# Performance work log

Hardware: AMD Instinct MI355X
Metric: run time of the kernel (lower is better)

## Reference

```python
import jax, jax.numpy as jnp
import numpy as np

E, T, H, I = 8, 2048, 1024, 2048  # experts, tokens, hidden, intermediate


def setup_inputs() -> dict:
    key = jax.random.key(0)
    k1, k2, k3, k4, k5 = jax.random.split(key, 5)
    hiddens = jax.random.normal(k1, (T, H), dtype=jnp.float32)
    w1 = jax.random.normal(k2, (E, H, I), dtype=jnp.float32)  # gate proj
    w2 = jax.random.normal(k3, (E, I, H), dtype=jnp.float32)  # down proj
    w3 = jax.random.normal(k4, (E, H, I), dtype=jnp.float32)  # up proj
    # random partition of T tokens into E contiguous expert groups (sum == T)
    cuts = jnp.sort(jax.random.randint(k5, (E - 1,), 0, T + 1, dtype=jnp.int32))
    bounds = jnp.concatenate(
        [jnp.zeros((1,), jnp.int32), cuts, jnp.full((1,), T, jnp.int32)])
    batch_sizes = jnp.diff(bounds)  # [E], int32, sums to T
    return {"hiddens": hiddens, "w1_weight": w1, "w2_weight": w2,
            "w3_weight": w3, "batch_sizes": batch_sizes}


def reference(hiddens, w1_weight, w2_weight, w3_weight, batch_sizes):
    # grouped GEMM: tokens are contiguous per expert; group_sizes = batch_sizes
    up = jax.lax.ragged_dot(hiddens, w1_weight, batch_sizes)      # [T, I]
    up_r = jax.lax.ragged_dot(hiddens, w3_weight, batch_sizes)    # [T, I]
    gated = jax.nn.silu(up) * up_r                                # SiLU-gate fuse
    down = jax.lax.ragged_dot(gated, w2_weight, batch_sizes)      # [T, H]
    return down
```

## Files before the change

### kernel.cpp

```cpp
#include <hip/hip_runtime.h>
#include <hip/hip_bf16.h>
#include <stdint.h>


#define NE 8
#define NT 2048
#define NH 1024
#define NI 2048

typedef __attribute__((ext_vector_type(8))) short bh8;
typedef __attribute__((ext_vector_type(4))) short bh4;
typedef __attribute__((ext_vector_type(4))) float f32x4;
typedef __attribute__((ext_vector_type(2))) float f32x2;
typedef __attribute__((ext_vector_type(4))) float float4v;

#define BARRIER() asm volatile("s_waitcnt lgkmcnt(0)\n\ts_barrier" ::: "memory")

static __device__ __forceinline__ unsigned short f2bf(float f) {
  __hip_bfloat16 h = __float2bfloat16(f);
  return *reinterpret_cast<unsigned short*>(&h);
}

__global__ __launch_bounds__(256)
void cvt_h_kernel(const float* __restrict__ x, unsigned short* __restrict__ y) {
  int i = blockIdx.x * 256 + threadIdx.x;
  const float4v* xv = reinterpret_cast<const float4v*>(x);
  float4v a = xv[2 * i], b = xv[2 * i + 1];
  union { bh8 v; unsigned short u[8]; } o;
  o.u[0] = f2bf(a[0]); o.u[1] = f2bf(a[1]); o.u[2] = f2bf(a[2]); o.u[3] = f2bf(a[3]);
  o.u[4] = f2bf(b[0]); o.u[5] = f2bf(b[1]); o.u[6] = f2bf(b[2]); o.u[7] = f2bf(b[3]);
  reinterpret_cast<bh8*>(y)[i] = o.v;
}


__global__ __launch_bounds__(512, 2)
void moe_gemm1(const unsigned short* __restrict__ hb,
               const float* __restrict__ w1,
               const float* __restrict__ w3,
               const int* __restrict__ bsz,
               unsigned short* __restrict__ gated) {
  const int NWG = 2048;
  const int wg = (blockIdx.x & 7) * (NWG >> 3) + (blockIdx.x >> 3);
  const int mt = wg & 15;
  const int e = (wg >> 4) & 7;
  const int nt = wg >> 7;

  int off = 0;
#pragma unroll
  for (int j = 0; j < NE; ++j) { int v = bsz[j]; off += (j < e) ? v : 0; }
  const int te = bsz[e];
  if (mt * 128 >= te) return;

  const int tid = threadIdx.x;
  const int l = tid & 63, w = tid >> 6;
  const int wr = w >> 2, wc = w & 3;

  __shared__ __align__(16) unsigned short As[2][128 * 32];
  __shared__ __align__(16) unsigned short B1s[2][128 * 32];
  __shared__ __align__(16) unsigned short B3s[2][128 * 32];

  const int row0 = off + mt * 128;
  const int col0 = nt * 128;

  int gr = row0 + (tid >> 2); if (gr > NT - 1) gr = NT - 1;
  const unsigned short* agA = hb + (size_t)gr * NH + (tid & 3) * 8;
  const int awo = (tid >> 2) * 32 + (((tid & 3) ^ ((tid >> 3) & 3)) * 8);

  const int n0 = 2 * l;
  const float* w1p = w1 + (size_t)e * NH * NI + (size_t)(4 * w) * NI + (col0 + n0);
  const float* w3p = w3 + (size_t)e * NH * NI + (size_t)(4 * w) * NI + (col0 + n0);
  const int bwo = n0 * 32 + (((w >> 1) ^ (l & 3)) * 8) + (w & 1) * 4;

  const int arow = wr * 64 + (l & 15);
  const int fslA = ((l >> 4) ^ ((l >> 1) & 3)) * 8;
  const int nbase = wc * 32 + (l & 15);
  const int bsl = ((l >> 4) ^ ((nbase >> 1) & 3)) * 8;

  f32x4 acc1[4][2] = {};
  f32x4 acc3[4][2] = {};
  f32x2 rb1A[4], rb3A[4], rb1B[4], rb3B[4];
  bh8 rAA, rAB;

  auto issue = [&](int t, bh8& rA_, f32x2 (&rb1_)[4], f32x2 (&rb3_)[4]) {
    const int k0 = t * 32;
    rA_ = *(const bh8*)(agA + k0);
#pragma unroll
    for (int j = 0; j < 4; ++j) rb1_[j] = *(const f32x2*)(w1p + (size_t)(k0 + j) * NI);
#pragma unroll
    for (int j = 0; j < 4; ++j) rb3_[j] = *(const f32x2*)(w3p + (size_t)(k0 + j) * NI);
  };
  auto stage = [&](int b, bh8& rA_, f32x2 (&rb1_)[4], f32x2 (&rb3_)[4]) {
    *(bh8*)(&As[b][awo]) = rA_;
    bh4 q0, q1, r0, r1;
#pragma unroll
    for (int j = 0; j < 4; ++j) {
      q0[j] = (short)f2bf(rb1_[j][0]); q1[j] = (short)f2bf(rb1_[j][1]);
      r0[j] = (short)f2bf(rb3_[j][0]); r1[j] = (short)f2bf(rb3_[j][1]);
    }
    *(bh4*)(&B1s[b][bwo]) = q0;
    *(bh4*)(&B1s[b][bwo + 32]) = q1;
    *(bh4*)(&B3s[b][bwo]) = r0;
    *(bh4*)(&B3s[b][bwo + 32]) = r1;
  };
  auto mfma_step = [&](int b) {
    bh8 af[4];
#pragma unroll
    for (int m = 0; m < 4; ++m)
      af[m] = *(const bh8*)(&As[b][(arow + m * 16) * 32 + fslA]);
#pragma unroll
    for (int nf = 0; nf < 2; ++nf) {
      bh8 b1f = *(const bh8*)(&B1s[b][(nbase + nf * 16) * 32 + bsl]);
      bh8 b3f = *(const bh8*)(&B3s[b][(nbase + nf * 16) * 32 + bsl]);
#pragma unroll
      for (int m = 0; m < 4; ++m) {
        acc1[m][nf] = __builtin_amdgcn_mfma_f32_16x16x32_bf16(af[m], b1f, acc1[m][nf], 0, 0, 0);
        acc3[m][nf] = __builtin_amdgcn_mfma_f32_16x16x32_bf16(af[m], b3f, acc3[m][nf], 0, 0, 0);
      }
    }
  };

  issue(0, rAA, rb1A, rb3A);
  issue(1, rAB, rb1B, rb3B);
  stage(0, rAA, rb1A, rb3A);
  BARRIER();

#pragma unroll 1
  for (int u = 0; u < 16; ++u) {
    const int t0 = 2 * u;
    if (t0 + 2 < 32) issue(t0 + 2, rAA, rb1A, rb3A);
    mfma_step(0);
    stage(1, rAB, rb1B, rb3B);
    BARRIER();
    if (t0 + 3 < 32) issue(t0 + 3, rAB, rb1B, rb3B);
    mfma_step(1);
    if (t0 + 2 < 32) stage(0, rAA, rb1A, rb3A);
    BARRIER();
  }

#pragma unroll
  for (int m = 0; m < 4; ++m) {
#pragma unroll
    for (int r = 0; r < 4; ++r) {
      int trow = mt * 128 + wr * 64 + m * 16 + (l >> 4) * 4 + r;
      if (trow < te) {
        size_t base = (size_t)(off + trow) * NI + col0 + wc * 32 + (l & 15);
#pragma unroll
        for (int nf = 0; nf < 2; ++nf) {
          float u2 = acc1[m][nf][r];
          float g = acc3[m][nf][r];
          gated[base + nf * 16] = f2bf((u2 / (1.f + __expf(-u2))) * g);
        }
      }
    }
  }
}

__global__ __launch_bounds__(512, 2)
void moe_gemm2(const unsigned short* __restrict__ gated,
               const float* __restrict__ w2,
               const int* __restrict__ bsz,
               float* __restrict__ out) {
  const int NWG = 1024;
  const int wg = (blockIdx.x & 7) * (NWG >> 3) + (blockIdx.x >> 3);
  const int mt = wg & 15;
  const int e = (wg >> 4) & 7;
  const int nt = wg >> 7;

  int off = 0;
#pragma unroll
  for (int j = 0; j < NE; ++j) { int v = bsz[j]; off += (j < e) ? v : 0; }
  const int te = bsz[e];
  if (mt * 128 >= te) return;

  const int tid = threadIdx.x;
  const int l = tid & 63, w = tid >> 6;
  const int wr = w >> 2, wc = w & 3;

  __shared__ __align__(16) unsigned short As[2][128 * 32];
  __shared__ __align__(16) unsigned short Bs[2][128 * 32];

  const int row0 = off + mt * 128;
  const int col0 = nt * 128;

  int gr = row0 + (tid >> 2); if (gr > NT - 1) gr = NT - 1;
  const unsigned short* agA = gated + (size_t)gr * NI + (tid & 3) * 8;
  const int awo = (tid >> 2) * 32 + (((tid & 3) ^ ((tid >> 3) & 3)) * 8);

  const int n0 = 2 * l;
  const float* w2p = w2 + (size_t)e * NI * NH + (size_t)(4 * w) * NH + (col0 + n0);
  const int bwo = n0 * 32 + (((w >> 1) ^ (l & 3)) * 8) + (w & 1) * 4;

  const int arow = wr * 64 + (l & 15);
  const int fslA = ((l >> 4) ^ ((l >> 1) & 3)) * 8;
  const int nbase = wc * 32 + (l & 15);
  const int bsl = ((l >> 4) ^ ((nbase >> 1) & 3)) * 8;

  f32x4 acc[4][2] = {};
  f32x2 rbA[4], rbB[4];
  bh8 rAA, rAB;

  auto issue = [&](int t, bh8& rA_, f32x2 (&rb_)[4]) {
    const int k0 = t * 32;
    rA_ = *(const bh8*)(agA + k0);
#pragma unroll
    for (int j = 0; j < 4; ++j) rb_[j] = *(const f32x2*)(w2p + (size_t)(k0 + j) * NH);
  };
  auto stage = [&](int b, bh8& rA_, f32x2 (&rb_)[4]) {
    *(bh8*)(&As[b][awo]) = rA_;
    bh4 q0, q1;
#pragma unroll
    for (int j = 0; j < 4; ++j) {
      q0[j] = (short)f2bf(rb_[j][0]); q1[j] = (short)f2bf(rb_[j][1]);
    }
    *(bh4*)(&Bs[b][bwo]) = q0;
    *(bh4*)(&Bs[b][bwo + 32]) = q1;
  };
  auto mfma_step = [&](int b) {
    bh8 af[4];
#pragma unroll
    for (int m = 0; m < 4; ++m)
      af[m] = *(const bh8*)(&As[b][(arow + m * 16) * 32 + fslA]);
#pragma unroll
    for (int nf = 0; nf < 2; ++nf) {
      bh8 bf = *(const bh8*)(&Bs[b][(nbase + nf * 16) * 32 + bsl]);
#pragma unroll
      for (int m = 0; m < 4; ++m)
        acc[m][nf] = __builtin_amdgcn_mfma_f32_16x16x32_bf16(af[m], bf, acc[m][nf], 0, 0, 0);
    }
  };

  issue(0, rAA, rbA);
  issue(1, rAB, rbB);
  stage(0, rAA, rbA);
  BARRIER();

#pragma unroll 1
  for (int u = 0; u < 32; ++u) {
    const int t0 = 2 * u;
    if (t0 + 2 < 64) issue(t0 + 2, rAA, rbA);
    mfma_step(0);
    stage(1, rAB, rbB);
    BARRIER();
    if (t0 + 3 < 64) issue(t0 + 3, rAB, rbB);
    mfma_step(1);
    if (t0 + 2 < 64) stage(0, rAA, rbA);
    BARRIER();
  }

#pragma unroll
  for (int m = 0; m < 4; ++m) {
#pragma unroll
    for (int r = 0; r < 4; ++r) {
      int trow = mt * 128 + wr * 64 + m * 16 + (l >> 4) * 4 + r;
      if (trow < te) {
        size_t base = (size_t)(off + trow) * NH + col0 + wc * 32 + (l & 15);
#pragma unroll
        for (int nf = 0; nf < 2; ++nf)
          out[base + nf * 16] = acc[m][nf][r];
      }
    }
  }
}

extern "C" void kernel_launch(void* const* d_in, const int* in_sizes, int n_in,
                              void* d_out, int out_size, void* d_ws, size_t ws_size,
                              hipStream_t stream) {
  const float* hiddens = (const float*)d_in[0];
  const float* w1 = (const float*)d_in[1];
  const float* w2 = (const float*)d_in[2];
  const float* w3 = (const float*)d_in[3];
  const int* bsz = (const int*)d_in[4];
  float* out = (float*)d_out;

  unsigned short* hb = (unsigned short*)d_ws;
  unsigned short* gated = hb + (size_t)NT * NH;

  cvt_h_kernel<<<dim3(NT * NH / 8 / 256), dim3(256), 0, stream>>>(hiddens, hb);
  moe_gemm1<<<dim3(2048), dim3(512), 0, stream>>>(hb, w1, w3, bsz, gated);
  moe_gemm2<<<dim3(1024), dim3(512), 0, stream>>>(gated, w2, bsz, out);
}
```

Before: 135.0 us.

## Deepen register prefetch pipeline to four stages and raise MFMA wave priority

Both grouped-GEMM kernels now keep four K-tiles of global loads in flight in registers instead of two, rotating through four register sets with an unrolled four-phase loop. The aim is to hide more global memory latency for the fp32 weight streams. The MFMA sections are also wrapped in s_setprio so matrix work is favoured over other waves' memory issue. The extra register sets raise VGPR pressure, which may cut occupancy or cause spills, especially in the gate/up kernel.

Result: no change. 133.1 us (-1.4%).

```diff
diff --git a/kernel.cpp b/kernel.cpp
--- a/kernel.cpp
+++ b/kernel.cpp
@@ -78,8 +78,9 @@
 
   f32x4 acc1[4][2] = {};
   f32x4 acc3[4][2] = {};
-  f32x2 rb1A[4], rb3A[4], rb1B[4], rb3B[4];
-  bh8 rAA, rAB;
+  bh8 rA0, rA1, rA2, rA3;
+  f32x2 r10[4], r11[4], r12[4], r13[4];
+  f32x2 r30[4], r31[4], r32[4], r33[4];
 
   auto issue = [&](int t, bh8& rA_, f32x2 (&rb1_)[4], f32x2 (&rb3_)[4]) {
     const int k0 = t * 32;
@@ -107,6 +108,7 @@
 #pragma unroll
     for (int m = 0; m < 4; ++m)
       af[m] = *(const bh8*)(&As[b][(arow + m * 16) * 32 + fslA]);
+    __builtin_amdgcn_s_setprio(1);
 #pragma unroll
     for (int nf = 0; nf < 2; ++nf) {
       bh8 b1f = *(const bh8*)(&B1s[b][(nbase + nf * 16) * 32 + bsl]);
@@ -117,25 +119,31 @@
         acc3[m][nf] = __builtin_amdgcn_mfma_f32_16x16x32_bf16(af[m], b3f, acc3[m][nf], 0, 0, 0);
       }
     }
-  };
-
-  issue(0, rAA, rb1A, rb3A);
-  issue(1, rAB, rb1B, rb3B);
-  stage(0, rAA, rb1A, rb3A);
+    __builtin_amdgcn_s_setprio(0);
+  };
+#define PHASE(P, RAI, R1I, R3I, RAS, R1S, R3S, LDSP)                    \
+  {                                                                     \
+    if ((P) + 4 < 32) issue((P) + 4, RAI, R1I, R3I);                    \
+    mfma_step(LDSP);                                                    \
+    if ((P) + 1 < 32) stage((LDSP) ^ 1, RAS, R1S, R3S);                 \
+    BARRIER();                                                          \
+  }
+
+  issue(0, rA0, r10, r30);
+  issue(1, rA1, r11, r31);
+  issue(2, rA2, r12, r32);
+  issue(3, rA3, r13, r33);
+  stage(0, rA0, r10, r30);
   BARRIER();
 
 #pragma unroll 1
-  for (int u = 0; u < 16; ++u) {
-    const int t0 = 2 * u;
-    if (t0 + 2 < 32) issue(t0 + 2, rAA, rb1A, rb3A);
-    mfma_step(0);
-    stage(1, rAB, rb1B, rb3B);
-    BARRIER();
-    if (t0 + 3 < 32) issue(t0 + 3, rAB, rb1B, rb3B);
-    mfma_step(1);
-    if (t0 + 2 < 32) stage(0, rAA, rb1A, rb3A);
-    BARRIER();
-  }
+  for (int p = 0; p < 32; p += 4) {
+    PHASE(p + 0, rA0, r10, r30, rA1, r11, r31, 0);
+    PHASE(p + 1, rA1, r11, r31, rA2, r12, r32, 1);
+    PHASE(p + 2, rA2, r12, r32, rA3, r13, r33, 0);
+    PHASE(p + 3, rA3, r13, r33, rA0, r10, r30, 1);
+  }
+#undef PHASE
 
 #pragma unroll
   for (int m = 0; m < 4; ++m) {
@@ -196,8 +204,8 @@
   const int bsl = ((l >> 4) ^ ((nbase >> 1) & 3)) * 8;
 
   f32x4 acc[4][2] = {};
-  f32x2 rbA[4], rbB[4];
-  bh8 rAA, rAB;
+  bh8 rA0, rA1, rA2, rA3;
+  f32x2 r0_[4], r1_[4], r2_[4], r3_[4];
 
   auto issue = [&](int t, bh8& rA_, f32x2 (&rb_)[4]) {
     const int k0 = t * 32;
@@ -220,6 +228,7 @@
 #pragma unroll
     for (int m = 0; m < 4; ++m)
       af[m] = *(const bh8*)(&As[b][(arow + m * 16) * 32 + fslA]);
+    __builtin_amdgcn_s_setprio(1);
 #pragma unroll
     for (int nf = 0; nf < 2; ++nf) {
       bh8 bf = *(const bh8*)(&Bs[b][(nbase + nf * 16) * 32 + bsl]);
@@ -227,25 +236,31 @@
       for (int m = 0; m < 4; ++m)
         acc[m][nf] = __builtin_amdgcn_mfma_f32_16x16x32_bf16(af[m], bf, acc[m][nf], 0, 0, 0);
     }
-  };
-
-  issue(0, rAA, rbA);
-  issue(1, rAB, rbB);
-  stage(0, rAA, rbA);
+    __builtin_amdgcn_s_setprio(0);
+  };
+#define PHASE2(P, RAI, RBI, RAS, RBS, LDSP)                             \
+  {                                                                     \
+    if ((P) + 4 < 64) issue((P) + 4, RAI, RBI);                         \
+    mfma_step(LDSP);                                                    \
+    if ((P) + 1 < 64) stage((LDSP) ^ 1, RAS, RBS);                      \
+    BARRIER();                                                          \
+  }
+
+  issue(0, rA0, r0_);
+  issue(1, rA1, r1_);
+  issue(2, rA2, r2_);
+  issue(3, rA3, r3_);
+  stage(0, rA0, r0_);
   BARRIER();
 
 #pragma unroll 1
-  for (int u = 0; u < 32; ++u) {
-    const int t0 = 2 * u;
-    if (t0 + 2 < 64) issue(t0 + 2, rAA, rbA);
-    mfma_step(0);
-    stage(1, rAB, rbB);
-    BARRIER();
-    if (t0 + 3 < 64) issue(t0 + 3, rAB, rbB);
-    mfma_step(1);
-    if (t0 + 2 < 64) stage(0, rAA, rbA);
-    BARRIER();
-  }
+  for (int p = 0; p < 64; p += 4) {
+    PHASE2(p + 0, rA0, r0_, rA1, r1_, 0);
+    PHASE2(p + 1, rA1, r1_, rA2, r2_, 1);
+    PHASE2(p + 2, rA2, r2_, rA3, r3_, 0);
+    PHASE2(p + 3, rA3, r3_, rA0, r0_, 1);
+  }
+#undef PHASE2
 
 #pragma unroll
   for (int m = 0; m < 4; ++m) {
```

## Split gate/up GEMM into separate workgroups and move SiLU-gate into down GEMM

Applied to the files above, without the earlier changes.

The first GEMM no longer computes both w1 and w3 products in one workgroup. It launches twice as many workgroups, each computing one projection and writing it unfused as bf16. The down-projection kernel now loads both intermediates and applies SiLU-gating while staging A into shared memory. This halves registers and LDS per workgroup in the up kernel, with s_setprio around MFMA blocks added. The cost is an extra T×I intermediate write and read, a second rounding to bf16 before the gate, and repeated exp work per down-projection column tile.

Measured after the change: 189.1 us. +40.1%, slower.

```diff
diff --git a/kernel.cpp b/kernel.cpp
--- a/kernel.cpp
+++ b/kernel.cpp
@@ -19,6 +19,9 @@
 static __device__ __forceinline__ unsigned short f2bf(float f) {
   __hip_bfloat16 h = __float2bfloat16(f);
   return *reinterpret_cast<unsigned short*>(&h);
+}
+static __device__ __forceinline__ float bf2f(short s) {
+  return __uint_as_float(((unsigned int)(unsigned short)s) << 16);
 }
 
 __global__ __launch_bounds__(256)
@@ -34,16 +37,18 @@
 
 
 __global__ __launch_bounds__(512, 2)
-void moe_gemm1(const unsigned short* __restrict__ hb,
-               const float* __restrict__ w1,
-               const float* __restrict__ w3,
-               const int* __restrict__ bsz,
-               unsigned short* __restrict__ gated) {
-  const int NWG = 2048;
+void moe_up(const unsigned short* __restrict__ hb,
+            const float* __restrict__ w1,
+            const float* __restrict__ w3,
+            const int* __restrict__ bsz,
+            unsigned short* __restrict__ up,
+            unsigned short* __restrict__ upr) {
+  const int NWG = 4096;
   const int wg = (blockIdx.x & 7) * (NWG >> 3) + (blockIdx.x >> 3);
   const int mt = wg & 15;
   const int e = (wg >> 4) & 7;
-  const int nt = wg >> 7;
+  const int which = (wg >> 7) & 1;
+  const int nt = wg >> 8;
 
   int off = 0;
 #pragma unroll
@@ -51,13 +56,15 @@
   const int te = bsz[e];
   if (mt * 128 >= te) return;
 
+  const float* W = which ? w3 : w1;
+  unsigned short* O = which ? upr : up;
+
   const int tid = threadIdx.x;
   const int l = tid & 63, w = tid >> 6;
   const int wr = w >> 2, wc = w & 3;
 
   __shared__ __align__(16) unsigned short As[2][128 * 32];
-  __shared__ __align__(16) unsigned short B1s[2][128 * 32];
-  __shared__ __align__(16) unsigned short B3s[2][128 * 32];
+  __shared__ __align__(16) unsigned short Bs[2][128 * 32];
 
   const int row0 = off + mt * 128;
   const int col0 = nt * 128;
@@ -67,8 +74,7 @@
   const int awo = (tid >> 2) * 32 + (((tid & 3) ^ ((tid >> 3) & 3)) * 8);
 
   const int n0 = 2 * l;
-  const float* w1p = w1 + (size_t)e * NH * NI + (size_t)(4 * w) * NI + (col0 + n0);
-  const float* w3p = w3 + (size_t)e * NH * NI + (size_t)(4 * w) * NI + (col0 + n0);
+  const float* wp = W + (size_t)e * NH * NI + (size_t)(4 * w) * NI + (col0 + n0);
   const int bwo = n0 * 32 + (((w >> 1) ^ (l & 3)) * 8) + (w & 1) * 4;
 
   const int arow = wr * 64 + (l & 15);
@@ -76,64 +82,57 @@
   const int nbase = wc * 32 + (l & 15);
   const int bsl = ((l >> 4) ^ ((nbase >> 1) & 3)) * 8;
 
-  f32x4 acc1[4][2] = {};
-  f32x4 acc3[4][2] = {};
-  f32x2 rb1A[4], rb3A[4], rb1B[4], rb3B[4];
-  bh8 rAA, rAB;
-
-  auto issue = [&](int t, bh8& rA_, f32x2 (&rb1_)[4], f32x2 (&rb3_)[4]) {
+  f32x4 acc[4][2] = {};
+  bh8 rA0, rA1;
+  f32x2 rb0[4], rb1[4];
+
+  auto issue = [&](int t, bh8& rA_, f32x2 (&rb_)[4]) {
     const int k0 = t * 32;
     rA_ = *(const bh8*)(agA + k0);
 #pragma unroll
-    for (int j = 0; j < 4; ++j) rb1_[j] = *(const f32x2*)(w1p + (size_t)(k0 + j) * NI);
-#pragma unroll
-    for (int j = 0; j < 4; ++j) rb3_[j] = *(const f32x2*)(w3p + (size_t)(k0 + j) * NI);
-  };
-  auto stage = [&](int b, bh8& rA_, f32x2 (&rb1_)[4], f32x2 (&rb3_)[4]) {
+    for (int j = 0; j < 4; ++j) rb_[j] = *(const f32x2*)(wp + (size_t)(k0 + j) * NI);
+  };
+  auto stage = [&](int b, bh8& rA_, f32x2 (&rb_)[4]) {
     *(bh8*)(&As[b][awo]) = rA_;
-    bh4 q0, q1, r0, r1;
+    bh4 q0, q1;
 #pragma unroll
     for (int j = 0; j < 4; ++j) {
-      q0[j] = (short)f2bf(rb1_[j][0]); q1[j] = (short)f2bf(rb1_[j][1]);
-      r0[j] = (short)f2bf(rb3_[j][0]); r1[j] = (short)f2bf(rb3_[j][1]);
-    }
-    *(bh4*)(&B1s[b][bwo]) = q0;
-    *(bh4*)(&B1s[b][bwo + 32]) = q1;
-    *(bh4*)(&B3s[b][bwo]) = r0;
-    *(bh4*)(&B3s[b][bwo + 32]) = r1;
+      q0[j] = (short)f2bf(rb_[j][0]); q1[j] = (short)f2bf(rb_[j][1]);
+    }
+    *(bh4*)(&Bs[b][bwo]) = q0;
+    *(bh4*)(&Bs[b][bwo + 32]) = q1;
   };
   auto mfma_step = [&](int b) {
     bh8 af[4];
 #pragma unroll
     for (int m = 0; m < 4; ++m)
       af[m] = *(const bh8*)(&As[b][(arow + m * 16) * 32 + fslA]);
+    __builtin_amdgcn_s_setprio(1);
 #pragma unroll
     for (int nf = 0; nf < 2; ++nf) {
-      bh8 b1f = *(const bh8*)(&B1s[b][(nbase + nf * 16) * 32 + bsl]);
-      bh8 b3f = *(const bh8*)(&B3s[b][(nbase + nf * 16) * 32 + bsl]);
-#pragma unroll
-      for (int m = 0; m < 4; ++m) {
-        acc1[m][nf] = __builtin_amdgcn_mfma_f32_16x16x32_bf16(af[m], b1f, acc1[m][nf], 0, 0, 0);
-        acc3[m][nf] = __builtin_amdgcn_mfma_f32_16x16x32_bf16(af[m], b3f, acc3[m][nf], 0, 0, 0);
-      }
-    }
-  };
-
-  issue(0, rAA, rb1A, rb3A);
-  issue(1, rAB, rb1B, rb3B);
-  stage(0, rAA, rb1A, rb3A);
+      bh8 bf = *(const bh8*)(&Bs[b][(nbase + nf * 16) * 32 + bsl]);
+#pragma unroll
+      for (int m = 0; m < 4; ++m)
+        acc[m][nf] = __builtin_amdgcn_mfma_f32_16x16x32_bf16(af[m], bf, acc[m][nf], 0, 0, 0);
+    }
+    __builtin_amdgcn_s_setprio(0);
+  };
+
+  issue(0, rA0, rb0);
+  issue(1, rA1, rb1);
+  stage(0, rA0, rb0);
   BARRIER();
 
 #pragma unroll 1
   for (int u = 0; u < 16; ++u) {
     const int t0 = 2 * u;
-    if (t0 + 2 < 32) issue(t0 + 2, rAA, rb1A, rb3A);
+    if (t0 + 2 < 32) issue(t0 + 2, rA0, rb0);
     mfma_step(0);
-    stage(1, rAB, rb1B, rb3B);
-    BARRIER();
-    if (t0 + 3 < 32) issue(t0 + 3, rAB, rb1B, rb3B);
+    stage(1, rA1, rb1);
+    BARRIER();
+    if (t0 + 3 < 32) issue(t0 + 3, rA1, rb1);
     mfma_step(1);
-    if (t0 + 2 < 32) stage(0, rAA, rb1A, rb3A);
+    if (t0 + 2 < 32) stage(0, rA0, rb0);
     BARRIER();
   }
 
@@ -145,21 +144,19 @@
       if (trow < te) {
         size_t base = (size_t)(off + trow) * NI + col0 + wc * 32 + (l & 15);
 #pragma unroll
-        for (int nf = 0; nf < 2; ++nf) {
-          float u2 = acc1[m][nf][r];
-          float g = acc3[m][nf][r];
-          gated[base + nf * 16] = f2bf((u2 / (1.f + __expf(-u2))) * g);
-        }
+        for (int nf = 0; nf < 2; ++nf)
+          O[base + nf * 16] = f2bf(acc[m][nf][r]);
       }
     }
   }
 }
 
 __global__ __launch_bounds__(512, 2)
-void moe_gemm2(const unsigned short* __restrict__ gated,
-               const float* __restrict__ w2,
-               const int* __restrict__ bsz,
-               float* __restrict__ out) {
+void moe_down(const unsigned short* __restrict__ up,
+              const unsigned short* __restrict__ upr,
+              const float* __restrict__ w2,
+              const int* __restrict__ bsz,
+              float* __restrict__ out) {
   const int NWG = 1024;
   const int wg = (blockIdx.x & 7) * (NWG >> 3) + (blockIdx.x >> 3);
   const int mt = wg & 15;
@@ -183,7 +180,9 @@
   const int col0 = nt * 128;
 
   int gr = row0 + (tid >> 2); if (gr > NT - 1) gr = NT - 1;
-  const unsigned short* agA = gated + (size_t)gr * NI + (tid & 3) * 8;
+  const size_t aoff = (size_t)gr * NI + (tid & 3) * 8;
+  const unsigned short* agU = up + aoff;
+  const unsigned short* agR = upr + aoff;
   const int awo = (tid >> 2) * 32 + (((tid & 3) ^ ((tid >> 3) & 3)) * 8);
 
   const int n0 = 2 * l;
@@ -196,17 +195,25 @@
   const int bsl = ((l >> 4) ^ ((nbase >> 1) & 3)) * 8;
 
   f32x4 acc[4][2] = {};
-  f32x2 rbA[4], rbB[4];
-  bh8 rAA, rAB;
-
-  auto issue = [&](int t, bh8& rA_, f32x2 (&rb_)[4]) {
+  bh8 rU0, rU1, rR0, rR1;
+  f32x2 rb0[4], rb1[4];
+
+  auto issue = [&](int t, bh8& rU_, bh8& rR_, f32x2 (&rb_)[4]) {
     const int k0 = t * 32;
-    rA_ = *(const bh8*)(agA + k0);
+    rU_ = *(const bh8*)(agU + k0);
+    rR_ = *(const bh8*)(agR + k0);
 #pragma unroll
     for (int j = 0; j < 4; ++j) rb_[j] = *(const f32x2*)(w2p + (size_t)(k0 + j) * NH);
   };
-  auto stage = [&](int b, bh8& rA_, f32x2 (&rb_)[4]) {
-    *(bh8*)(&As[b][awo]) = rA_;
+  auto stage = [&](int b, bh8& rU_, bh8& rR_, f32x2 (&rb_)[4]) {
+    union { bh8 v; unsigned short u[8]; } ga;
+#pragma unroll
+    for (int j = 0; j < 8; ++j) {
+      float u2 = bf2f(rU_[j]);
+      float g = bf2f(rR_[j]);
+      ga.u[j] = f2bf((u2 / (1.f + __expf(-u2))) * g);
+    }
+    *(bh8*)(&As[b][awo]) = ga.v;
     bh4 q0, q1;
 #pragma unroll
     for (int j = 0; j < 4; ++j) {
@@ -220,6 +227,7 @@
 #pragma unroll
     for (int m = 0; m < 4; ++m)
       af[m] = *(const bh8*)(&As[b][(arow + m * 16) * 32 + fslA]);
+    __builtin_amdgcn_s_setprio(1);
 #pragma unroll
     for (int nf = 0; nf < 2; ++nf) {
       bh8 bf = *(const bh8*)(&Bs[b][(nbase + nf * 16) * 32 + bsl]);
@@ -227,23 +235,24 @@
       for (int m = 0; m < 4; ++m)
         acc[m][nf] = __builtin_amdgcn_mfma_f32_16x16x32_bf16(af[m], bf, acc[m][nf], 0, 0, 0);
     }
-  };
-
-  issue(0, rAA, rbA);
-  issue(1, rAB, rbB);
-  stage(0, rAA, rbA);
+    __builtin_amdgcn_s_setprio(0);
+  };
+
+  issue(0, rU0, rR0, rb0);
+  issue(1, rU1, rR1, rb1);
+  stage(0, rU0, rR0, rb0);
   BARRIER();
 
 #pragma unroll 1
   for (int u = 0; u < 32; ++u) {
     const int t0 = 2 * u;
-    if (t0 + 2 < 64) issue(t0 + 2, rAA, rbA);
+    if (t0 + 2 < 64) issue(t0 + 2, rU0, rR0, rb0);
     mfma_step(0);
-    stage(1, rAB, rbB);
-    BARRIER();
-    if (t0 + 3 < 64) issue(t0 + 3, rAB, rbB);
+    stage(1, rU1, rR1, rb1);
+    BARRIER();
+    if (t0 + 3 < 64) issue(t0 + 3, rU1, rR1, rb1);
     mfma_step(1);
-    if (t0 + 2 < 64) stage(0, rAA, rbA);
+    if (t0 + 2 < 64) stage(0, rU0, rR0, rb0);
     BARRIER();
   }
 
@@ -273,9 +282,10 @@
   float* out = (float*)d_out;
 
   unsigned short* hb = (unsigned short*)d_ws;
-  unsigned short* gated = hb + (size_t)NT * NH;
+  unsigned short* up = hb + (size_t)NT * NH;
+  unsigned short* upr = up + (size_t)NT * NI;
 
   cvt_h_kernel<<<dim3(NT * NH / 8 / 256), dim3(256), 0, stream>>>(hiddens, hb);
-  moe_gemm1<<<dim3(2048), dim3(512), 0, stream>>>(hb, w1, w3, bsz, gated);
-  moe_gemm2<<<dim3(1024), dim3(512), 0, stream>>>(gated, w2, bsz, out);
-}
+  moe_up<<<dim3(4096), dim3(512), 0, stream>>>(hb, w1, w3, bsz, up, upr);
+  moe_down<<<dim3(1024), dim3(512), 0, stream>>>(up, upr, w2, bsz, out);
+}
```
